# Kernel optimization log

Measured on AMD Instinct MI355X. Metric: run time of the kernel, lower is better.

The kernel has to match this reference:

```python
import jax, jax.numpy as jnp
import numpy as np

G = 8           # graphs
NBG = 1024      # blocks per graph
APB = 4         # atoms per block
NC = 1          # coord channels
HID = 512
ES = 64
K = 9
L = 3
NLVL = 50
NB = G * NBG
NU = NB * APB
NUM_BLOCK, NUM_ATOM, NUM_POS = 25, 16, 16
BIG = 1e9


def _cumsum_ids(seg_lengths, n):
    # faithful to torch: zeros, mark segment starts via cumsum(lengths)[:-1], cumsum
    ids = jnp.zeros((n,), jnp.int32).at[jnp.cumsum(seg_lengths)[:-1]].set(1)
    return jnp.cumsum(ids)


def setup_inputs() -> dict:
    key = jax.random.key(0)
    ks = jax.random.split(key, 18)
    s = 0.02
    return {
        'Z': 3.0 * jax.random.normal(ks[0], (NU, NC, 3), jnp.float32),
        'B': jax.random.randint(ks[1], (NB,), 0, NUM_BLOCK),
        'A': jax.random.randint(ks[2], (NU,), 0, NUM_ATOM),
        'atom_positions': jax.random.randint(ks[3], (NU,), 0, NUM_POS),
        'block_lengths': jnp.full((NB,), APB, jnp.int32),
        'lengths': jnp.full((G,), NBG, jnp.int32),
        'segment_ids': jax.random.randint(ks[4], (NB,), 0, 2),
        'noise': jax.random.normal(ks[5], (NU, NC, 3), jnp.float32),
        'noise_level': jax.random.randint(ks[6], (G,), 0, NLVL),
        'sigmas': jnp.asarray(np.exp(np.linspace(np.log(10.0), np.log(0.01), NLVL)), jnp.float32),
        'atom_emb': s * jax.random.normal(ks[7], (NUM_ATOM, HID), jnp.float32),
        'pos_emb': s * jax.random.normal(ks[8], (NUM_POS, HID), jnp.float32),
        'block_emb': s * jax.random.normal(ks[9], (NUM_BLOCK, HID), jnp.float32),
        'edge_emb': s * jax.random.normal(ks[10], (2, ES), jnp.float32),
        'Wm': s * jax.random.normal(ks[11], (L, HID, HID), jnp.float32),
        'We': s * jax.random.normal(ks[12], (L, ES, HID), jnp.float32),
        'Wu': s * jax.random.normal(ks[13], (L, HID, HID), jnp.float32),
        'wz': s * jax.random.normal(ks[14], (L, HID), jnp.float32),
        'W1': s * jax.random.normal(ks[15], (HID, HID), jnp.float32),
        'b1': jnp.zeros((HID,), jnp.float32),
        'W2': s * jax.random.normal(ks[16], (HID, 1), jnp.float32),
    }


def _forward(Z, B, A, atom_positions, block_lengths, lengths, segment_ids,
             noise, noise_level, sigmas, atom_emb, pos_emb, block_emb, edge_emb,
             Wm, We, Wu, wz, W1, b1, W2):
    nb, nu, g = B.shape[0], A.shape[0], lengths.shape[0]
    nbg, apb = nb // g, nu // nb
    batch_id = _cumsum_ids(lengths, nb)        # [Nb]
    block_id = _cumsum_ids(block_lengths, nu)  # [Nu]

    # perturb: Z + noise * sigma[noise_level[graph]]
    used = sigmas[noise_level][batch_id][block_id]          # [Nu]
    Zp = Z + noise * used[:, None, None]                    # [Nu, NC, 3]

    # block embedding: atom + position + block-type
    H0 = atom_emb[A] + pos_emb[atom_positions] + block_emb[B][block_id]  # [Nu, H]

    # edges: fully connect -> split intra/inter by segment -> knn by min atom-pair distance
    xa = Zp.reshape(g, nbg * apb * NC, 3)
    sq = jnp.sum(xa * xa, axis=-1)
    d2 = sq[:, :, None] + sq[:, None, :] - 2.0 * jnp.einsum('gnd,gmd->gnm', xa, xa)
    D = d2.reshape(g, nbg, apb * NC, nbg, apb * NC).min(axis=(2, 4))     # [g, nbg, nbg]
    seg = segment_ids.reshape(g, nbg)
    same = seg[:, :, None] == seg[:, None, :]
    eye = jnp.eye(nbg, dtype=bool)[None]
    _, idx_intra = jax.lax.top_k(-jnp.where(same & ~eye, D, BIG), K)     # [g, nbg, K]
    _, idx_inter = jax.lax.top_k(-jnp.where(~same, D, BIG), K)
    off = (jnp.arange(g, dtype=jnp.int32) * nbg)[:, None, None]
    dst_loc = jnp.broadcast_to(jnp.arange(nbg, dtype=jnp.int32)[None, :, None] + off, (g, nbg, K))
    src = jnp.concatenate([(idx_intra + off).reshape(-1), (idx_inter + off).reshape(-1)])
    dst = jnp.concatenate([dst_loc.reshape(-1), dst_loc.reshape(-1)])
    eattr = edge_emb[jnp.concatenate([jnp.zeros(g * nbg * K, jnp.int32), jnp.ones(g * nbg * K, jnp.int32)])]

    # encoder (GET surrogate): block-level equivariant message passing
    h = jax.ops.segment_sum(H0, block_id, num_segments=nb) / apb                    # [Nb, H]
    Zb0 = jax.ops.segment_sum(Zp.mean(axis=1), block_id, num_segments=nb) / apb    # [Nb, 3]
    Zb = Zb0
    for l in range(Wm.shape[0]):
        m = jax.nn.silu((h[src] + h[dst]) @ Wm[l] + eattr @ We[l])                  # [E, H]
        h = h + jax.nn.silu(jax.ops.segment_sum(m, dst, num_segments=nb) @ Wu[l])
        coef = jnp.tanh(m @ wz[l])                                                  # [E]
        Zb = Zb + jax.ops.segment_sum((Zb[src] - Zb[dst]) * coef[:, None], dst, num_segments=nb) / (2 * K)
    pred_Z = Zp + (Zb - Zb0)[block_id][:, None, :]
    unit_repr = H0 + h[block_id]
    block_repr = h
    graph_repr = jax.ops.segment_sum(h, batch_id, num_segments=g)

    # energy head: SiLU -> Linear -> SiLU -> Linear(no bias), summed per graph
    e = jax.nn.silu(jax.nn.silu(block_repr) @ W1 + b1) @ W2                         # [Nb, 1]
    pred_energy = jax.ops.segment_sum(e[:, 0], batch_id, num_segments=g)            # [g]

    pred_noise = pred_Z - Zp
    per_unit = jnp.sum((pred_noise - noise) ** 2, axis=(-1, -2))                    # [Nu]
    nl = jax.ops.segment_sum(per_unit, batch_id[block_id], num_segments=g)
    loss = 0.5 * nl.mean()
    return pred_energy, pred_noise, unit_repr, block_repr, graph_repr, loss


def reference(Z, B, A, atom_positions, block_lengths, lengths, segment_ids,
              noise, noise_level, sigmas, atom_emb, pos_emb, block_emb, edge_emb,
              Wm, We, Wu, wz, W1, b1, W2):
    return _forward(Z, B, A, atom_positions, block_lengths, lengths, segment_ids,
                    noise, noise_level, sigmas, atom_emb, pos_emb, block_emb, edge_emb,
                    Wm, We, Wu, wz, W1, b1, W2)
```

## Files before the change

### kernel.cpp

```cpp
#include <hip/hip_runtime.h>
#include <hip/hip_bf16.h>

typedef __bf16 bf16;
typedef __bf16 bf16x2 __attribute__((ext_vector_type(2)));
typedef __bf16 bf16x8 __attribute__((ext_vector_type(8)));
typedef float floatx4 __attribute__((ext_vector_type(4)));

#define NB_ 8192
#define NU_ 32768

__device__ __forceinline__ float silu_f(float x) {
    float e = __expf(-x);
    return x * __builtin_amdgcn_rcpf(1.0f + e);
}

__device__ __forceinline__ float2 unpack_bf2(unsigned v) {
    float2 r;
    r.x = __uint_as_float(v << 16);
    r.y = __uint_as_float(v & 0xFFFF0000u);
    return r;
}

__device__ __forceinline__ void gll16(const bf16* g, bf16* l) {
    __builtin_amdgcn_global_load_lds((const __attribute__((address_space(1))) void*)g,
                                     (__attribute__((address_space(3))) void*)l, 16, 0, 0);
}

__global__ __launch_bounds__(256) void init_kernel(
    const float* __restrict__ Z, const float* __restrict__ noise,
    const int* __restrict__ nl, const float* __restrict__ sig,
    const int* __restrict__ Aarr, const int* __restrict__ posa, const int* __restrict__ Barr,
    const float* __restrict__ atom_emb, const float* __restrict__ pos_emb,
    const float* __restrict__ block_emb,
    const float* __restrict__ edge_emb, const float* __restrict__ We,
    const float* __restrict__ Wm, const float* __restrict__ Wu, const float* __restrict__ W1,
    float* __restrict__ Zp, float* __restrict__ Zb0, float* __restrict__ Zb,
    float* __restrict__ hf, bf16* __restrict__ hb,
    bf16* __restrict__ WmT, bf16* __restrict__ WuT, bf16* __restrict__ W1T,
    float* __restrict__ ebias,
    float* __restrict__ out_gr, float* __restrict__ eblk, float* __restrict__ out_loss)
{
    __shared__ float zsh[12];
    __shared__ float tile[32][33];
    int bid = blockIdx.x, tid = threadIdx.x;
    if (bid < 8192) {
        int b = bid, g = b >> 10;
        if (tid < 12) {
            float sg = sig[nl[g]];
            int idx = b*12 + tid;
            float zp = Z[idx] + noise[idx]*sg;
            Zp[idx] = zp;
            zsh[tid] = zp;
        }
        __syncthreads();
        if (tid < 3) {
            float v = 0.25f*(zsh[tid] + zsh[3+tid] + zsh[6+tid] + zsh[9+tid]);
            Zb0[b*3+tid] = v; Zb[b*3+tid] = v;
        }
        int ai[4], pi[4];
        #pragma unroll
        for (int a = 0; a < 4; a++) { ai[a] = Aarr[b*4+a]*512; pi[a] = posa[b*4+a]*512; }
        int bb = Barr[b]*512;
        #pragma unroll
        for (int cc = 0; cc < 2; cc++) {
            int c = tid + cc*256;
            float s = 0.0f;
            #pragma unroll
            for (int a = 0; a < 4; a++) s += atom_emb[ai[a]+c] + pos_emb[pi[a]+c];
            s = 0.25f*s + block_emb[bb+c];
            hf[(size_t)b*512+c] = s;
            hb[(size_t)b*512+c] = (bf16)s;
        }
        return;
    }
    bid -= 8192;
    if (bid < 1792) {
        int z = bid >> 8, rem = bid & 255;
        int bx = rem & 15, by = rem >> 4;
        int tx = tid & 31, ty = tid >> 5;
        const float* src; bf16* dst;
        if (z < 3)      { src = Wm + (size_t)z*262144;     dst = WmT + (size_t)z*262144; }
        else if (z < 6) { src = Wu + (size_t)(z-3)*262144; dst = WuT + (size_t)(z-3)*262144; }
        else            { src = W1;                        dst = W1T; }
        #pragma unroll
        for (int i = 0; i < 32; i += 8)
            tile[ty+i][tx] = src[(size_t)(by*32+ty+i)*512 + bx*32+tx];
        __syncthreads();
        #pragma unroll
        for (int i = 0; i < 32; i += 8)
            dst[(size_t)(bx*32+ty+i)*512 + by*32+tx] = (bf16)tile[tx][ty+i];
        return;
    }
    bid -= 1792;
    if (bid < 12) {
        int gid = bid*256 + tid;
        int l = gid >> 10, t = (gid >> 9) & 1, c = gid & 511;
        float s = 0.0f;
        #pragma unroll 8
        for (int e = 0; e < 64; e++)
            s += edge_emb[t*64 + e] * We[(size_t)(l*64 + e)*512 + c];
        ebias[gid] = s;
        return;
    }
    bid -= 12;
    int k = bid*256 + tid;
    if (k < 4096) out_gr[k] = 0.0f;
    else if (k < 12288) eblk[k-4096] = 0.0f;
    else if (k == 12288) out_loss[0] = 0.0f;
}

__device__ void knn_body(int kb, const float* __restrict__ Zp, const int* __restrict__ seg,
                         int* __restrict__ nbr) {
    int wid = threadIdx.x >> 6;
    int lane = threadIdx.x & 63;
    int r = ((kb & 7) << 10) + ((kb >> 3) << 2) + wid;
    int g = r >> 10;
    int il = r & 1023;
    int base = g << 10;
    int segr = seg[r];
    float za[4][3];
    #pragma unroll
    for (int a = 0; a < 4; a++)
        #pragma unroll
        for (int d = 0; d < 3; d++)
            za[a][d] = Zp[r*12 + a*3 + d];
    float dist[16];
    unsigned smask = 0;
    #pragma unroll
    for (int t = 0; t < 16; t++) {
        int jb = base + t*64 + lane;
        const float4* p = (const float4*)(Zp + (size_t)jb*12);
        float4 v0 = p[0], v1 = p[1], v2 = p[2];
        float bx[4] = {v0.x, v0.w, v1.z, v2.y};
        float by[4] = {v0.y, v1.x, v1.w, v2.z};
        float bz[4] = {v0.z, v1.y, v2.x, v2.w};
        float dm = 3.0e38f;
        #pragma unroll
        for (int a = 0; a < 4; a++) {
            #pragma unroll
            for (int bq = 0; bq < 4; bq++) {
                float dx = za[a][0]-bx[bq], dy = za[a][1]-by[bq], dz = za[a][2]-bz[bq];
                dm = fminf(dm, dx*dx + dy*dy + dz*dz);
            }
        }
        dist[t] = dm;
        if (seg[jb] == segr) smask |= (1u << t);
    }
    const float INF = 3.0e38f;
    for (int phase = 0; phase < 2; phase++) {
        float wd[16];
        #pragma unroll
        for (int t = 0; t < 16; t++) {
            bool ok = (phase == 0) ? (((smask >> t) & 1u) && (t*64 + lane != il))
                                   : (!((smask >> t) & 1u));
            wd[t] = ok ? dist[t] : INF;
        }
        for (int it = 0; it < 9; it++) {
            float bd = wd[0]; int bt = 0;
            #pragma unroll
            for (int t = 1; t < 16; t++) { if (wd[t] < bd) { bd = wd[t]; bt = t; } }
            float mv = bd;
            #pragma unroll
            for (int off = 32; off >= 1; off >>= 1) mv = fminf(mv, __shfl_xor(mv, off, 64));
            unsigned long long msk = __ballot(bd == mv);
            int wl = __ffsll(msk) - 1;
            int wt = __shfl(bt, wl, 64);
            if (lane == 0) nbr[r*18 + phase*9 + it] = base + wt*64 + wl;
            bool amwin = (lane == wl);
            #pragma unroll
            for (int t = 0; t < 16; t++) if (amwin && t == wt) wd[t] = INF;
        }
    }
}

__device__ void gemm_body(const bf16* __restrict__ A, const bf16* __restrict__ BT,
                          bf16* __restrict__ Pb, float* __restrict__ hf,
                          bf16* __restrict__ hb, bf16* __restrict__ shp,
                          const float* __restrict__ b1, const float* __restrict__ W2,
                          float* __restrict__ eblk,
                          float* __restrict__ Zb, const float* __restrict__ zacc,
                          int mode, int bid)
{
    __shared__ alignas(16) bf16 sA[128*32];
    __shared__ alignas(16) bf16 sB[64*32];
    int mt = bid & 63, nt = bid >> 6;
    int m0 = mt*128, n0 = nt*64;
    int tid = threadIdx.x, lane = tid & 63, w = tid >> 6;
    int wm = w & 1, wn = w >> 1;
    int lm = lane & 15, q = lane >> 4;

    int pA0 = w*128 + lane, pA1 = pA0 + 64, pB = w*64 + lane;
    int rA0 = pA0 >> 2, qA0 = (pA0 & 3) ^ ((rA0 >> 1) & 3);
    int rA1 = pA1 >> 2, qA1 = (pA1 & 3) ^ ((rA1 >> 1) & 3);
    int rB  = pB  >> 2, qB  = (pB  & 3) ^ ((rB  >> 1) & 3);
    const bf16* gA0 = A  + (size_t)(m0 + rA0)*512 + qA0*8;
    const bf16* gA1 = A  + (size_t)(m0 + rA1)*512 + qA1*8;
    const bf16* gB  = BT + (size_t)(n0 + rB )*512 + qB*8;
    bf16* lA0 = sA + (w*128)*8;
    bf16* lA1 = sA + (w*128 + 64)*8;
    bf16* lB  = sB + (w*64)*8;

    int swq = (q ^ ((lm >> 1) & 3)) * 8;
    const bf16* pa[4]; const bf16* pb2[2];
    #pragma unroll
    for (int tm = 0; tm < 4; tm++) pa[tm] = sA + (wm*64 + tm*16 + lm)*32 + swq;
    #pragma unroll
    for (int tn = 0; tn < 2; tn++) pb2[tn] = sB + (wn*32 + tn*16 + lm)*32 + swq;

    floatx4 zv = {0.0f, 0.0f, 0.0f, 0.0f};
    floatx4 acc[4][2];
    #pragma unroll
    for (int i = 0; i < 4; i++)
        #pragma unroll
        for (int j = 0; j < 2; j++) acc[i][j] = zv;

    for (int k0 = 0; k0 < 512; k0 += 32) {
        gll16(gA0 + k0, lA0);
        gll16(gA1 + k0, lA1);
        gll16(gB  + k0, lB);
        __syncthreads();
        bf16x8 af[4], bfr[2];
        #pragma unroll
        for (int tm = 0; tm < 4; tm++) af[tm] = *(const bf16x8*)pa[tm];
        #pragma unroll
        for (int tn = 0; tn < 2; tn++) bfr[tn] = *(const bf16x8*)pb2[tn];
        #pragma unroll
        for (int tm = 0; tm < 4; tm++)
            #pragma unroll
            for (int tn = 0; tn < 2; tn++)
                acc[tm][tn] = __builtin_amdgcn_mfma_f32_16x16x32_bf16(af[tm], bfr[tn], acc[tm][tn], 0, 0, 0);
        __syncthreads();
    }

    if (mode == 1 && nt == 0) {
        int o = m0*3 + tid;
        Zb[o] += zacc[o] * (1.0f/18.0f);
        if (tid < 128) {
            int o2 = m0*3 + 256 + tid;
            Zb[o2] += zacc[o2] * (1.0f/18.0f);
        }
    }

    if (mode == 2) {
        #pragma unroll
        for (int tm = 0; tm < 4; tm++) {
            #pragma unroll
            for (int rr = 0; rr < 4; rr++) {
                float part = 0.0f;
                #pragma unroll
                for (int tn = 0; tn < 2; tn++) {
                    int col = n0 + wn*32 + tn*16 + lm;
                    float t = silu_f(acc[tm][tn][rr] + b1[col]);
                    part += t * W2[col];
                }
                part += __shfl_xor(part, 1, 64);
                part += __shfl_xor(part, 2, 64);
                part += __shfl_xor(part, 4, 64);
                part += __shfl_xor(part, 8, 64);
                if (lm == 0) {
                    int row = m0 + wm*64 + tm*16 + q*4 + rr;
                    atomicAdd(&eblk[row], part);
                }
            }
        }
        return;
    }
    #pragma unroll
    for (int tm = 0; tm < 4; tm++) {
        #pragma unroll
        for (int tn = 0; tn < 2; tn++) {
            #pragma unroll
            for (int rr = 0; rr < 4; rr++) {
                int row = m0 + wm*64 + tm*16 + q*4 + rr;
                int col = n0 + wn*32 + tn*16 + lm;
                size_t o = (size_t)row*512 + col;
                float v = acc[tm][tn][rr];
                if (mode == 0) {
                    Pb[o] = (bf16)v;
                } else {
                    float nh = hf[o] + silu_f(v);
                    hf[o] = nh;
                    hb[o] = (bf16)nh;
                    if (shp) shp[o] = (bf16)silu_f(nh);
                }
            }
        }
    }
}

__global__ __launch_bounds__(256) void gemm_kernel(const bf16* __restrict__ A, const bf16* __restrict__ BT,
                                                   bf16* __restrict__ Pb, float* __restrict__ hf,
                                                   bf16* __restrict__ hb, bf16* __restrict__ shp,
                                                   const float* __restrict__ b1, const float* __restrict__ W2,
                                                   float* __restrict__ eblk,
                                                   float* __restrict__ Zb, const float* __restrict__ zacc,
                                                   int mode) {
    gemm_body(A, BT, Pb, hf, hb, shp, b1, W2, eblk, Zb, zacc, mode, blockIdx.x);
}

__global__ __launch_bounds__(256) void knn_pgemm0_kernel(const bf16* __restrict__ hb,
                                                         const bf16* __restrict__ WmT0,
                                                         bf16* __restrict__ Pb,
                                                         const float* __restrict__ Zp,
                                                         const int* __restrict__ seg,
                                                         int* __restrict__ nbr) {
    if (blockIdx.x < 512)
        gemm_body(hb, WmT0, Pb, nullptr, nullptr, nullptr, nullptr, nullptr, nullptr,
                  nullptr, nullptr, 0, blockIdx.x);
    else
        knn_body(blockIdx.x - 512, Zp, seg, nbr);
}

__global__ __launch_bounds__(256) void edge_kernel(const bf16* __restrict__ Pb, const float* __restrict__ ebias,
                                                   const float* __restrict__ wz, const float* __restrict__ Zb,
                                                   const int* __restrict__ nbr, bf16* __restrict__ msum,
                                                   float* __restrict__ zacc) {
    int bid = blockIdx.x, tid = threadIdx.x;
    int b = ((bid & 7) << 10) | (bid >> 3);
    int c0 = 2*tid;
    int lane = tid & 63, wid = tid >> 6;
    __shared__ int srcs[18];
    __shared__ float red[18][4];
    __shared__ float term[18][3];
    if (tid < 18) srcs[tid] = nbr[b*18 + tid];
    __syncthreads();
    float2 pd  = unpack_bf2(*(const unsigned*)(Pb + (size_t)b*512 + c0));
    float2 eb0 = *(const float2*)(ebias + c0);
    float2 eb1 = *(const float2*)(ebias + 512 + c0);
    float2 w   = *(const float2*)(wz + c0);
    float ms0 = 0.0f, ms1 = 0.0f;
    float pdot[18];
    #pragma unroll
    for (int e = 0; e < 18; e++) {
        int s = srcs[e];
        float2 pv = unpack_bf2(*(const unsigned*)(Pb + (size_t)s*512 + c0));
        float ba = (e < 9) ? eb0.x : eb1.x;
        float bb = (e < 9) ? eb0.y : eb1.y;
        float m0 = silu_f(pv.x + pd.x + ba);
        float m1 = silu_f(pv.y + pd.y + bb);
        ms0 += m0; ms1 += m1;
        pdot[e] = m0*w.x + m1*w.y;
    }
    bf16x2 mp = { (bf16)ms0, (bf16)ms1 };
    *(bf16x2*)(msum + (size_t)b*512 + c0) = mp;
    #pragma unroll
    for (int e = 0; e < 18; e++) {
        float v = pdot[e];
        #pragma unroll
        for (int off = 32; off >= 1; off >>= 1) v += __shfl_xor(v, off, 64);
        if (lane == 0) red[e][wid] = v;
    }
    __syncthreads();
    if (tid < 18) {
        float dot = red[tid][0] + red[tid][1] + red[tid][2] + red[tid][3];
        float coef = tanhf(dot);
        int s = srcs[tid];
        #pragma unroll
        for (int d = 0; d < 3; d++)
            term[tid][d] = (Zb[s*3 + d] - Zb[b*3 + d]) * coef;
    }
    __syncthreads();
    if (tid < 3) {
        float s = 0.0f;
        #pragma unroll
        for (int e = 0; e < 18; e++) s += term[e][tid];
        zacc[b*3 + tid] = s;
    }
}

__global__ __launch_bounds__(256) void finalize_kernel(const float* __restrict__ eblk, float* __restrict__ out_e,
                                                       const float* __restrict__ hf, float* __restrict__ out_gr,
                                                       const float* __restrict__ Zb, const float* __restrict__ Zb0,
                                                       const float* __restrict__ noise,
                                                       float* __restrict__ out_pn, float* __restrict__ out_loss) {
    __shared__ float red[256];
    int bid = blockIdx.x, tid = threadIdx.x;
    if (bid < 8) {
        int g = bid;
        float s = 0.0f;
        #pragma unroll
        for (int k = 0; k < 4; k++) s += eblk[g*1024 + k*256 + tid];
        red[tid] = s; __syncthreads();
        for (int st = 128; st > 0; st >>= 1) {
            if (tid < st) red[tid] += red[tid+st];
            __syncthreads();
        }
        if (tid == 0) out_e[g] = red[0];
        return;
    }
    if (bid < 136) {
        int u = (bid-8)*256 + tid;
        int b = u >> 2;
        float per = 0.0f;
        #pragma unroll
        for (int d = 0; d < 3; d++) {
            float dv = Zb[b*3+d] - Zb0[b*3+d];
            out_pn[u*3+d] = dv;
            float e = dv - noise[u*3+d];
            per += e*e;
        }
        red[tid] = per; __syncthreads();
        for (int st = 128; st > 0; st >>= 1) {
            if (tid < st) red[tid] += red[tid+st];
            __syncthreads();
        }
        if (tid == 0) atomicAdd(out_loss, red[0] * (1.0f/16.0f));
        return;
    }
    int pid = bid - 136;
    int g = pid >> 5;
    int rc = (pid >> 1) & 15;
    int ch = pid & 1;
    int c = ch*256 + tid;
    int b0 = (g << 10) + rc*64;
    float s = 0.0f;
    for (int i = 0; i < 64; i++) s += hf[(size_t)(b0+i)*512 + c];
    atomicAdd(&out_gr[g*512 + c], s);
}

__global__ __launch_bounds__(256) void unitrepr_kernel(const int* __restrict__ Aarr, const int* __restrict__ posa,
                                                       const int* __restrict__ Barr,
                                                       const float* __restrict__ atom_emb, const float* __restrict__ pos_emb,
                                                       const float* __restrict__ block_emb,
                                                       const float* __restrict__ hf, float* __restrict__ out_ur) {
    int gid = blockIdx.x*256 + threadIdx.x;
    int u = gid >> 7, c = (gid & 127) << 2, b = u >> 2;
    float4 va = *(const float4*)(atom_emb + (size_t)Aarr[u]*512 + c);
    float4 vp = *(const float4*)(pos_emb + (size_t)posa[u]*512 + c);
    float4 vb = *(const float4*)(block_emb + (size_t)Barr[b]*512 + c);
    float4 vh = *(const float4*)(hf + (size_t)b*512 + c);
    float4 o;
    o.x = va.x + vp.x + vb.x + vh.x;
    o.y = va.y + vp.y + vb.y + vh.y;
    o.z = va.z + vp.z + vb.z + vh.z;
    o.w = va.w + vp.w + vb.w + vh.w;
    *(float4*)(out_ur + (size_t)u*512 + c) = o;
}

extern "C" void kernel_launch(void* const* d_in, const int* in_sizes, int n_in,
                              void* d_out, int out_size, void* d_ws, size_t ws_size,
                              hipStream_t stream) {
    const float* Z         = (const float*)d_in[0];
    const int*   B         = (const int*)d_in[1];
    const int*   A         = (const int*)d_in[2];
    const int*   ap        = (const int*)d_in[3];
    const int*   seg       = (const int*)d_in[6];
    const float* noise     = (const float*)d_in[7];
    const int*   nl        = (const int*)d_in[8];
    const float* sig       = (const float*)d_in[9];
    const float* atom_emb  = (const float*)d_in[10];
    const float* pos_emb   = (const float*)d_in[11];
    const float* block_emb = (const float*)d_in[12];
    const float* edge_emb  = (const float*)d_in[13];
    const float* Wm        = (const float*)d_in[14];
    const float* We        = (const float*)d_in[15];
    const float* Wu        = (const float*)d_in[16];
    const float* wz        = (const float*)d_in[17];
    const float* W1        = (const float*)d_in[18];
    const float* b1        = (const float*)d_in[19];
    const float* W2        = (const float*)d_in[20];
    (void)in_sizes; (void)n_in; (void)d_ws; (void)ws_size; (void)out_size;

    float* out = (float*)d_out;
    const size_t o1 = 8, o2 = 98312, o3 = 16875528, o4 = 21069832, o5 = 21073928;
    float* out_e    = out;
    float* out_pn   = out + o1;
    float* out_ur   = out + o2;
    float* hf       = out + o3;
    float* out_gr   = out + o4;
    float* out_loss = out + o5;

    char* arena = (char*)(out + o2);
    bf16*  Pb   = (bf16*)(arena);
    bf16*  msum = (bf16*)(arena + 16777216);
    bf16*  sh   = (bf16*)(arena + 25165824);
    bf16*  hb   = (bf16*)(arena + 33554432);
    float* Zp   = (float*)(arena + 41943040);
    float* Zb0  = (float*)(arena + 42336256);
    float* Zb   = (float*)(arena + 42434560);
    float* zacc = (float*)(arena + 42532864);
    int*   nbr  = (int*)  (arena + 42631168);
    bf16*  WmT  = (bf16*) (arena + 43220992);
    bf16*  WuT  = (bf16*) (arena + 44793856);
    bf16*  W1T  = (bf16*) (arena + 46366720);
    float* ebias= (float*)(arena + 46891008);
    float* eblk = (float*)(arena + 46903296);

    init_kernel<<<8192 + 1792 + 12 + 49, 256, 0, stream>>>(
        Z, noise, nl, sig, A, ap, B, atom_emb, pos_emb, block_emb,
        edge_emb, We, Wm, Wu, W1,
        Zp, Zb0, Zb, hf, hb, WmT, WuT, W1T, ebias, out_gr, eblk, out_loss);

    knn_pgemm0_kernel<<<512 + 2048, 256, 0, stream>>>(hb, WmT, Pb, Zp, seg, nbr);

    for (int l = 0; l < 3; l++) {
        if (l > 0)
            gemm_kernel<<<512, 256, 0, stream>>>(hb, WmT + (size_t)l*262144, Pb,
                                                 nullptr, nullptr, nullptr, nullptr, nullptr, nullptr,
                                                 nullptr, nullptr, 0);
        edge_kernel<<<8192, 256, 0, stream>>>(Pb, ebias + l*1024, wz + l*512, Zb, nbr, msum, zacc);
        gemm_kernel<<<512, 256, 0, stream>>>(msum, WuT + (size_t)l*262144, nullptr,
                                             hf, hb, (l == 2) ? sh : nullptr, nullptr, nullptr, nullptr,
                                             Zb, zacc, 1);
    }
    gemm_kernel<<<512, 256, 0, stream>>>(sh, W1T, nullptr, nullptr, nullptr, nullptr,
                                         b1, W2, eblk, nullptr, nullptr, 2);
    finalize_kernel<<<392, 256, 0, stream>>>(eblk, out_e, hf, out_gr, Zb, Zb0, noise, out_pn, out_loss);
    unitrepr_kernel<<<16384, 256, 0, stream>>>(A, ap, B, atom_emb, pos_emb, block_emb, hf, out_ur);
}
```

Baseline: 491.0 us.

## Reduce energy head directly per graph and use DPP wave-min in kNN selection

The energy-head GEMM epilogue now sums silu outputs times W2 over the whole tile and issues one atomic per block straight into the per-graph energy, instead of per-row atomics into a block-energy buffer. This removes the eblk buffer, its zeroing, and the finalize stage that reduced it. The kNN top-k loop replaces the shuffle-xor min reduction and argmin tracking with a min tree, DPP row operations plus readlane, and a ballot scan to find the winning slot. The price is 16 ballots per iteration and a change in the order of floating-point summation.

```diff
diff --git a/kernel.cpp b/kernel.cpp
--- a/kernel.cpp
+++ b/kernel.cpp
@@ -24,6 +24,25 @@
 __device__ __forceinline__ void gll16(const bf16* g, bf16* l) {
     __builtin_amdgcn_global_load_lds((const __attribute__((address_space(1))) void*)g,
                                      (__attribute__((address_space(3))) void*)l, 16, 0, 0);
+}
+
+__device__ __forceinline__ float wave_min_bcast(float v) {
+    const int infi = __float_as_int(3.0e38f);
+    int vi = __float_as_int(v);
+    int t;
+    t  = __builtin_amdgcn_update_dpp(infi, vi, 0x111, 0xf, 0xf, false);
+    vi = __float_as_int(fminf(__int_as_float(vi), __int_as_float(t)));
+    t  = __builtin_amdgcn_update_dpp(infi, vi, 0x112, 0xf, 0xf, false);
+    vi = __float_as_int(fminf(__int_as_float(vi), __int_as_float(t)));
+    t  = __builtin_amdgcn_update_dpp(infi, vi, 0x114, 0xf, 0xf, false);
+    vi = __float_as_int(fminf(__int_as_float(vi), __int_as_float(t)));
+    t  = __builtin_amdgcn_update_dpp(infi, vi, 0x118, 0xf, 0xf, false);
+    vi = __float_as_int(fminf(__int_as_float(vi), __int_as_float(t)));
+    t  = __builtin_amdgcn_update_dpp(infi, vi, 0x142, 0xa, 0xf, false);
+    vi = __float_as_int(fminf(__int_as_float(vi), __int_as_float(t)));
+    t  = __builtin_amdgcn_update_dpp(infi, vi, 0x143, 0xc, 0xf, false);
+    vi = __float_as_int(fminf(__int_as_float(vi), __int_as_float(t)));
+    return __int_as_float(__builtin_amdgcn_readlane(vi, 63));
 }
 
 __global__ __launch_bounds__(256) void init_kernel(
@@ -38,7 +57,7 @@
     float* __restrict__ hf, bf16* __restrict__ hb,
     bf16* __restrict__ WmT, bf16* __restrict__ WuT, bf16* __restrict__ W1T,
     float* __restrict__ ebias,
-    float* __restrict__ out_gr, float* __restrict__ eblk, float* __restrict__ out_loss)
+    float* __restrict__ out_gr, float* __restrict__ out_e, float* __restrict__ out_loss)
 {
     __shared__ float zsh[12];
     __shared__ float tile[32][33];
@@ -105,8 +124,8 @@
     bid -= 12;
     int k = bid*256 + tid;
     if (k < 4096) out_gr[k] = 0.0f;
-    else if (k < 12288) eblk[k-4096] = 0.0f;
-    else if (k == 12288) out_loss[0] = 0.0f;
+    else if (k < 4104) out_e[k-4096] = 0.0f;
+    else if (k == 4104) out_loss[0] = 0.0f;
 }
 
 __device__ void knn_body(int kb, const float* __restrict__ Zp, const int* __restrict__ seg,
@@ -156,19 +175,28 @@
             wd[t] = ok ? dist[t] : INF;
         }
         for (int it = 0; it < 9; it++) {
-            float bd = wd[0]; int bt = 0;
-            #pragma unroll
-            for (int t = 1; t < 16; t++) { if (wd[t] < bd) { bd = wd[t]; bt = t; } }
-            float mv = bd;
-            #pragma unroll
-            for (int off = 32; off >= 1; off >>= 1) mv = fminf(mv, __shfl_xor(mv, off, 64));
-            unsigned long long msk = __ballot(bd == mv);
-            int wl = __ffsll(msk) - 1;
-            int wt = __shfl(bt, wl, 64);
+            float a0 = fminf(fminf(wd[0],  wd[1]),  wd[2]);
+            float a1 = fminf(fminf(wd[3],  wd[4]),  wd[5]);
+            float a2 = fminf(fminf(wd[6],  wd[7]),  wd[8]);
+            float a3 = fminf(fminf(wd[9],  wd[10]), wd[11]);
+            float a4 = fminf(fminf(wd[12], wd[13]), wd[14]);
+            float b0 = fminf(fminf(a0, a1), a2);
+            float b1v = fminf(fminf(a3, a4), wd[15]);
+            float mv = wave_min_bcast(fminf(b0, b1v));
+            int wt = -1; unsigned long long wm = 0ull;
+            #pragma unroll
+            for (int t = 0; t < 16; t++) {
+                unsigned long long bm = __ballot(wd[t] == mv);
+                bool take = (wt < 0) && (bm != 0ull);
+                wt = take ? t : wt;
+                wm = take ? bm : wm;
+            }
+            int wl = __ffsll(wm) - 1;
             if (lane == 0) nbr[r*18 + phase*9 + it] = base + wt*64 + wl;
-            bool amwin = (lane == wl);
-            #pragma unroll
-            for (int t = 0; t < 16; t++) if (amwin && t == wt) wd[t] = INF;
+            bool mine = (lane == wl);
+            #pragma unroll
+            for (int t = 0; t < 16; t++)
+                if (t == wt && mine) wd[t] = INF;
         }
     }
 }
@@ -177,7 +205,7 @@
                           bf16* __restrict__ Pb, float* __restrict__ hf,
                           bf16* __restrict__ hb, bf16* __restrict__ shp,
                           const float* __restrict__ b1, const float* __restrict__ W2,
-                          float* __restrict__ eblk,
+                          float* __restrict__ out_e,
                           float* __restrict__ Zb, const float* __restrict__ zacc,
                           int mode, int bid)
 {
@@ -242,26 +270,26 @@
     }
 
     if (mode == 2) {
-        #pragma unroll
-        for (int tm = 0; tm < 4; tm++) {
-            #pragma unroll
-            for (int rr = 0; rr < 4; rr++) {
-                float part = 0.0f;
+        float esum = 0.0f;
+        #pragma unroll
+        for (int tn = 0; tn < 2; tn++) {
+            int col = n0 + wn*32 + tn*16 + lm;
+            float bb = b1[col];
+            float w2 = W2[col];
+            #pragma unroll
+            for (int tm = 0; tm < 4; tm++)
                 #pragma unroll
-                for (int tn = 0; tn < 2; tn++) {
-                    int col = n0 + wn*32 + tn*16 + lm;
-                    float t = silu_f(acc[tm][tn][rr] + b1[col]);
-                    part += t * W2[col];
-                }
-                part += __shfl_xor(part, 1, 64);
-                part += __shfl_xor(part, 2, 64);
-                part += __shfl_xor(part, 4, 64);
-                part += __shfl_xor(part, 8, 64);
-                if (lm == 0) {
-                    int row = m0 + wm*64 + tm*16 + q*4 + rr;
-                    atomicAdd(&eblk[row], part);
-                }
-            }
+                for (int rr = 0; rr < 4; rr++)
+                    esum += silu_f(acc[tm][tn][rr] + bb) * w2;
+        }
+        #pragma unroll
+        for (int off = 32; off >= 1; off >>= 1) esum += __shfl_xor(esum, off, 64);
+        __shared__ float ered[4];
+        if (lane == 0) ered[w] = esum;
+        __syncthreads();
+        if (tid == 0) {
+            float tot = ered[0] + ered[1] + ered[2] + ered[3];
+            atomicAdd(&out_e[m0 >> 10], tot);
         }
         return;
     }
@@ -292,10 +320,10 @@
                                                    bf16* __restrict__ Pb, float* __restrict__ hf,
                                                    bf16* __restrict__ hb, bf16* __restrict__ shp,
                                                    const float* __restrict__ b1, const float* __restrict__ W2,
-                                                   float* __restrict__ eblk,
+                                                   float* __restrict__ out_e,
                                                    float* __restrict__ Zb, const float* __restrict__ zacc,
                                                    int mode) {
-    gemm_body(A, BT, Pb, hf, hb, shp, b1, W2, eblk, Zb, zacc, mode, blockIdx.x);
+    gemm_body(A, BT, Pb, hf, hb, shp, b1, W2, out_e, Zb, zacc, mode, blockIdx.x);
 }
 
 __global__ __launch_bounds__(256) void knn_pgemm0_kernel(const bf16* __restrict__ hb,
@@ -368,28 +396,14 @@
     }
 }
 
-__global__ __launch_bounds__(256) void finalize_kernel(const float* __restrict__ eblk, float* __restrict__ out_e,
-                                                       const float* __restrict__ hf, float* __restrict__ out_gr,
+__global__ __launch_bounds__(256) void finalize_kernel(const float* __restrict__ hf, float* __restrict__ out_gr,
                                                        const float* __restrict__ Zb, const float* __restrict__ Zb0,
                                                        const float* __restrict__ noise,
                                                        float* __restrict__ out_pn, float* __restrict__ out_loss) {
     __shared__ float red[256];
     int bid = blockIdx.x, tid = threadIdx.x;
-    if (bid < 8) {
-        int g = bid;
-        float s = 0.0f;
-        #pragma unroll
-        for (int k = 0; k < 4; k++) s += eblk[g*1024 + k*256 + tid];
-        red[tid] = s; __syncthreads();
-        for (int st = 128; st > 0; st >>= 1) {
-            if (tid < st) red[tid] += red[tid+st];
-            __syncthreads();
-        }
-        if (tid == 0) out_e[g] = red[0];
-        return;
-    }
-    if (bid < 136) {
-        int u = (bid-8)*256 + tid;
+    if (bid < 128) {
+        int u = bid*256 + tid;
         int b = u >> 2;
         float per = 0.0f;
         #pragma unroll
@@ -407,7 +421,7 @@
         if (tid == 0) atomicAdd(out_loss, red[0] * (1.0f/16.0f));
         return;
     }
-    int pid = bid - 136;
+    int pid = bid - 128;
     int g = pid >> 5;
     int rc = (pid >> 1) & 15;
     int ch = pid & 1;
@@ -484,12 +498,11 @@
     bf16*  WuT  = (bf16*) (arena + 44793856);
     bf16*  W1T  = (bf16*) (arena + 46366720);
     float* ebias= (float*)(arena + 46891008);
-    float* eblk = (float*)(arena + 46903296);
-
-    init_kernel<<<8192 + 1792 + 12 + 49, 256, 0, stream>>>(
+
+    init_kernel<<<8192 + 1792 + 12 + 17, 256, 0, stream>>>(
         Z, noise, nl, sig, A, ap, B, atom_emb, pos_emb, block_emb,
         edge_emb, We, Wm, Wu, W1,
-        Zp, Zb0, Zb, hf, hb, WmT, WuT, W1T, ebias, out_gr, eblk, out_loss);
+        Zp, Zb0, Zb, hf, hb, WmT, WuT, W1T, ebias, out_gr, out_e, out_loss);
 
     knn_pgemm0_kernel<<<512 + 2048, 256, 0, stream>>>(hb, WmT, Pb, Zp, seg, nbr);
 
@@ -504,7 +517,7 @@
                                              Zb, zacc, 1);
     }
     gemm_kernel<<<512, 256, 0, stream>>>(sh, W1T, nullptr, nullptr, nullptr, nullptr,
-                                         b1, W2, eblk, nullptr, nullptr, 2);
-    finalize_kernel<<<392, 256, 0, stream>>>(eblk, out_e, hf, out_gr, Zb, Zb0, noise, out_pn, out_loss);
+                                         b1, W2, out_e, nullptr, nullptr, 2);
+    finalize_kernel<<<384, 256, 0, stream>>>(hf, out_gr, Zb, Zb0, noise, out_pn, out_loss);
     unitrepr_kernel<<<16384, 256, 0, stream>>>(A, ap, B, atom_emb, pos_emb, block_emb, hf, out_ur);
 }
```

Result: slower. 505.8 us (+3.0%).
